# Kernel tuning notes

Measured on AMD Instinct MI355X. Metric: run time of the kernel, lower is better.

The kernel has to match this reference:

```python
import jax, jax.numpy as jnp
import numpy as np

N_NODES = 100000
D_FEAT = 128
N_EDGES = 1600000
N_CLASSES = 32


def setup_inputs() -> dict:
    key = jax.random.key(0)
    k1, k2, k3, k4 = jax.random.split(key, 4)
    x = jax.random.normal(k1, (N_NODES, D_FEAT), dtype=jnp.float32)
    edge_index = jax.random.randint(k2, (2, N_EDGES), 0, N_NODES, dtype=jnp.int64)
    # Linear(input_feat, classes) params (PyTorch default init scale)
    bound = 1.0 / np.sqrt(D_FEAT)
    W = jax.random.uniform(k3, (N_CLASSES, D_FEAT), minval=-bound, maxval=bound, dtype=jnp.float32)
    b = jax.random.uniform(k4, (N_CLASSES,), minval=-bound, maxval=bound, dtype=jnp.float32)
    return {"x": x, "edge_index": edge_index, "W": W, "b": b}


def reference(x, edge_index, W, b):
    # GINConv: out = mlp((1 + eps) * x + sum_{j in N(i)} x_j), eps = 0 (default)
    src, dst = edge_index[0], edge_index[1]
    # gather source features [E, D] and scatter-add into target nodes [N, D]
    agg = jax.ops.segment_sum(x[src], dst, num_segments=N_NODES)
    h = x + agg  # (1 + eps) * x with eps = 0
    # Linear: [N, D] @ [D, C] + [C]
    return h @ W.T + b
```

## Files before the change

kernel.cpp:

```cpp
#include <hip/hip_runtime.h>

#define N_NODES 100000
#define D_FEAT 128
#define N_CLASSES 32
#define BSHIFT 8
#define NB 391
#define EPB 4096
#define CAPB 5120
#define GCAP 1536

typedef __attribute__((ext_vector_type(8))) short short8;
typedef __attribute__((ext_vector_type(4))) float f32x4;

__device__ __forceinline__ unsigned short f2bf(float f) {
  unsigned u = __float_as_uint(f);
  u += 0x7fffu + ((u >> 16) & 1);
  return (unsigned short)(u >> 16);
}

__global__ __launch_bounds__(256) void gin_prep(const float* __restrict__ W,
                                                unsigned short* __restrict__ Wb,
                                                int* __restrict__ gcount) {
  int i = blockIdx.x * 256 + threadIdx.x;
  if (i < D_FEAT * N_CLASSES) Wb[i] = f2bf(W[i]);
  if (i < NB) gcount[i] = 0;
}

__global__ __launch_bounds__(256) void gin_mid(
    const float* __restrict__ x, const unsigned short* __restrict__ Wb,
    float* __restrict__ y,
    const int* __restrict__ src, const int* __restrict__ dst,
    int* __restrict__ gcount, unsigned* __restrict__ bucketed,
    int E, int GBr) {
  __shared__ int cnt[NB];
  __shared__ int cur[NB];
  __shared__ int loff[NB + 1];
  __shared__ int gbase[NB];
  __shared__ int part[256];
  __shared__ unsigned sorted[EPB];
  int tid = threadIdx.x;

  if ((int)blockIdx.x >= GBr) {
    int pb = blockIdx.x - GBr;
    int wave = tid >> 6, lane = tid & 63;
    int node_base = pb * 64 + wave * 16;
    if (node_base >= N_NODES) return;
    int m = lane & 15, quad = lane >> 4;

    short8 bfrag[2][4];
#pragma unroll
    for (int cb = 0; cb < 2; ++cb) {
      const unsigned short* wr = Wb + (cb * 16 + m) * D_FEAT + quad * 8;
#pragma unroll
      for (int ks = 0; ks < 4; ++ks)
        bfrag[cb][ks] = *(const short8*)(wr + ks * 32);
    }

    const float* xr = x + (size_t)(node_base + m) * D_FEAT + quad * 8;
    short8 afrag[4];
#pragma unroll
    for (int ks = 0; ks < 4; ++ks) {
      float4 f0 = *(const float4*)(xr + ks * 32);
      float4 f1 = *(const float4*)(xr + ks * 32 + 4);
      float fl[8] = {f0.x, f0.y, f0.z, f0.w, f1.x, f1.y, f1.z, f1.w};
      short8 a;
#pragma unroll
      for (int j = 0; j < 8; ++j) a[j] = (short)f2bf(fl[j]);
      afrag[ks] = a;
    }

    f32x4 acc0 = {0.f, 0.f, 0.f, 0.f};
    f32x4 acc1 = {0.f, 0.f, 0.f, 0.f};
#pragma unroll
    for (int ks = 0; ks < 4; ++ks) {
      acc0 = __builtin_amdgcn_mfma_f32_16x16x32_bf16(afrag[ks], bfrag[0][ks], acc0, 0, 0, 0);
      acc1 = __builtin_amdgcn_mfma_f32_16x16x32_bf16(afrag[ks], bfrag[1][ks], acc1, 0, 0, 0);
    }

#pragma unroll
    for (int r = 0; r < 4; ++r) {
      int node = node_base + quad * 4 + r;
      y[(size_t)node * N_CLASSES + m] = acc0[r];
      y[(size_t)node * N_CLASSES + 16 + m] = acc1[r];
    }
    return;
  }

  int blk = blockIdx.x;
  for (int i = tid; i < NB; i += 256) {
    cnt[i] = 0;
    cur[i] = 0;
  }
  __syncthreads();
  int base = blk * EPB;
  bool full = (base + EPB <= E);

  int dv[16];
  unsigned sv[16];
  if (full) {
#pragma unroll
    for (int k = 0; k < 16; ++k) dv[k] = dst[base + k * 256 + tid];
#pragma unroll
    for (int k = 0; k < 16; ++k) sv[k] = (unsigned)src[base + k * 256 + tid];
  } else {
#pragma unroll
    for (int k = 0; k < 16; ++k) {
      int e = base + k * 256 + tid;
      dv[k] = (e < E) ? dst[e] : -1;
      sv[k] = (e < E) ? (unsigned)src[e] : 0u;
    }
  }
#pragma unroll
  for (int k = 0; k < 16; ++k)
    if (dv[k] >= 0) atomicAdd(&cnt[dv[k] >> BSHIFT], 1);
  __syncthreads();

  for (int i = tid; i < NB; i += 256) {
    int c = cnt[i];
    gbase[i] = c ? atomicAdd(&gcount[i], c) : 0;
  }
  int i0 = tid * 2;
  int v0 = (i0 < NB) ? cnt[i0] : 0;
  int v1 = (i0 + 1 < NB) ? cnt[i0 + 1] : 0;
  int s0 = v0 + v1;
  part[tid] = s0;
  __syncthreads();
  for (int o = 1; o < 256; o <<= 1) {
    int t = (tid >= o) ? part[tid - o] : 0;
    __syncthreads();
    part[tid] += t;
    __syncthreads();
  }
  int run = part[tid] - s0;
  if (i0 < NB) loff[i0] = run;
  if (i0 + 1 < NB) loff[i0 + 1] = run + v0;
  if (tid == 255) loff[NB] = part[255];
  __syncthreads();

#pragma unroll
  for (int k = 0; k < 16; ++k) {
    if (dv[k] >= 0) {
      int b = dv[k] >> BSHIFT;
      int r = atomicAdd(&cur[b], 1);
      sorted[loff[b] + r] = sv[k] | ((unsigned)(dv[k] & 255) << 17);
    }
  }
  __syncthreads();

  int ltot = loff[NB];
  for (int i = tid; i < ltot; i += 256) {
    int lo = 0, hi = NB;
    while (hi - lo > 1) {
      int md = (lo + hi) >> 1;
      if (loff[md] <= i) lo = md; else hi = md;
    }
    int ga = gbase[lo] + (i - loff[lo]);
    if (ga < CAPB) bucketed[(size_t)lo * CAPB + ga] = sorted[i];
  }
}

__global__ __launch_bounds__(512) void gin_gather_s(
    const int* __restrict__ gcount, const unsigned* __restrict__ bucketed,
    const float* __restrict__ y, const float* __restrict__ bias,
    float* __restrict__ out) {
  __shared__ unsigned sorted[GCAP];
  __shared__ int cnt[64];
  __shared__ int off[65];
  __shared__ int cur[64];
  int tid = threadIdx.x;
  int bk = blockIdx.x >> 2;
  int qq = blockIdx.x & 3;
  int len = gcount[bk];
  if (len > CAPB) len = CAPB;
  const unsigned* bb = bucketed + (size_t)bk * CAPB;
  if (tid < 64) cnt[tid] = 0;
  __syncthreads();
  for (int i = tid; i < len; i += 512) {
    unsigned p = bb[i];
    int n8 = (int)((p >> 17) & 255u);
    if ((n8 >> 6) == qq) atomicAdd(&cnt[n8 & 63], 1);
  }
  __syncthreads();
  if (tid == 0) off[0] = 0;
  if (tid < 64) off[tid + 1] = cnt[tid];
  __syncthreads();
  for (int o = 1; o < 64; o <<= 1) {
    int v = (tid < 64 && tid >= o) ? off[tid + 1 - o] : 0;
    __syncthreads();
    if (tid < 64) off[tid + 1] += v;
    __syncthreads();
  }
  if (tid < 64) cur[tid] = off[tid];
  __syncthreads();
  for (int i = tid; i < len; i += 512) {
    unsigned p = bb[i];
    int n8 = (int)((p >> 17) & 255u);
    if ((n8 >> 6) == qq) {
      int pos = atomicAdd(&cur[n8 & 63], 1);
      if (pos < GCAP) sorted[pos] = p;
    }
  }
  __syncthreads();
  int nl = tid >> 3;
  int q = tid & 7;
  int es = off[nl], ee = off[nl + 1];
  if (ee > GCAP) ee = GCAP;
  if (es > ee) es = ee;
  int node = (bk << 8) + (qq << 6) + nl;
  if (node >= N_NODES) return;
  const float4* y4 = (const float4*)y;
  float4 bq = ((const float4*)bias)[q];
  float4 self = y4[(size_t)node * 8 + q];
  float4 acc;
  acc.x = self.x + bq.x;
  acc.y = self.y + bq.y;
  acc.z = self.z + bq.z;
  acc.w = self.w + bq.w;
  int j = es;
  for (; j + 4 <= ee; j += 4) {
    unsigned s0 = sorted[j] & 0x1FFFF, s1 = sorted[j + 1] & 0x1FFFF;
    unsigned s2 = sorted[j + 2] & 0x1FFFF, s3 = sorted[j + 3] & 0x1FFFF;
    float4 w0 = y4[(size_t)s0 * 8 + q];
    float4 w1 = y4[(size_t)s1 * 8 + q];
    float4 w2 = y4[(size_t)s2 * 8 + q];
    float4 w3 = y4[(size_t)s3 * 8 + q];
    acc.x += w0.x + w1.x + w2.x + w3.x;
    acc.y += w0.y + w1.y + w2.y + w3.y;
    acc.z += w0.z + w1.z + w2.z + w3.z;
    acc.w += w0.w + w1.w + w2.w + w3.w;
  }
  for (; j < ee; ++j) {
    float4 w = y4[(size_t)(sorted[j] & 0x1FFFF) * 8 + q];
    acc.x += w.x; acc.y += w.y; acc.z += w.z; acc.w += w.w;
  }
  ((float4*)out)[(size_t)node * 8 + q] = acc;
}

__global__ __launch_bounds__(256) void gin_bias_init(
    const float* __restrict__ y, const float* __restrict__ b,
    float* __restrict__ out) {
  int gid = blockIdx.x * 256 + threadIdx.x;
  if (gid < N_NODES * N_CLASSES) out[gid] = y[gid] + b[gid & 31];
}
__global__ __launch_bounds__(256) void gin_scatter_fb(
    const int* __restrict__ src, const int* __restrict__ dst,
    const float* __restrict__ y, float* __restrict__ out, int n_edges) {
  long long gid = (long long)blockIdx.x * 256 + threadIdx.x;
  int e = (int)(gid >> 5);
  int c = (int)(gid & 31);
  if (e >= n_edges) return;
  atomicAdd(&out[(size_t)dst[e] * N_CLASSES + c],
            y[(size_t)src[e] * N_CLASSES + c]);
}

extern "C" void kernel_launch(void* const* d_in, const int* in_sizes, int n_in,
                              void* d_out, int out_size, void* d_ws, size_t ws_size,
                              hipStream_t stream) {
  const float* x = (const float*)d_in[0];
  const int* edge_index = (const int*)d_in[1];
  const float* W = (const float*)d_in[2];
  const float* b = (const float*)d_in[3];
  float* out = (float*)d_out;

  int E = in_sizes[1] / 2;
  const int* src = edge_index;
  const int* dst = edge_index + E;

  int GBr = (E + EPB - 1) / EPB;
  int pblocks = (N_NODES + 63) / 64;

  char* ws = (char*)d_ws;
  size_t sz_y = (size_t)N_NODES * N_CLASSES * 4;
  size_t sz_wb = (D_FEAT * N_CLASSES * 2 + 15) & ~15ull;
  size_t sz_bucketed = (((size_t)NB * CAPB * 4) + 15) & ~15ull;
  size_t sz_gcnt = ((size_t)NB * 4 + 15) & ~15ull;

  float* y = (float*)ws;
  unsigned short* Wb = (unsigned short*)(ws + sz_y);
  unsigned* bucketed = (unsigned*)(ws + sz_y + sz_wb);
  int* gcount = (int*)(ws + sz_y + sz_wb + sz_bucketed);
  size_t need = sz_y + sz_wb + sz_bucketed + sz_gcnt;

  bool dense = E > 1750000;

  if (ws_size < need || dense) {
    gin_prep<<<16, 256, 0, stream>>>(W, Wb, (int*)ws);
    gin_mid<<<pblocks, 256, 0, stream>>>(x, Wb, y, src, dst, (int*)ws, (unsigned*)ws, E, 0);
    gin_bias_init<<<(N_NODES * N_CLASSES + 255) / 256, 256, 0, stream>>>(y, b, out);
    long long t2 = (long long)E * N_CLASSES;
    gin_scatter_fb<<<(int)((t2 + 255) / 256), 256, 0, stream>>>(src, dst, y, out, E);
    return;
  }

  gin_prep<<<16, 256, 0, stream>>>(W, Wb, gcount);
  gin_mid<<<GBr + pblocks, 256, 0, stream>>>(x, Wb, y, src, dst, gcount, bucketed, E, GBr);
  gin_gather_s<<<NB * 4, 512, 0, stream>>>(gcount, bucketed, y, b, out);
}
```

Baseline: 155.7 us.

## Scatter bucketed edges directly, stage bucket in LDS, use packed bf16 convert

The bucketing kernel drops its local prefix-sum, LDS sort and binary-search copy-out. Each edge is now written straight to its global bucket slot using the per-block base plus its atomic rank, which cuts barriers and LDS use but makes the global writes less coalesced. The gather kernel keeps the bucket in a 20KB LDS stage buffer so its second pass does not re-read global memory, at the cost of more LDS per block and possibly lower occupancy. The projection path replaces the software float-to-bf16 rounding with the hardware packed convert instruction.

```diff
diff --git a/kernel.cpp b/kernel.cpp
--- a/kernel.cpp
+++ b/kernel.cpp
@@ -18,6 +18,12 @@
   return (unsigned short)(u >> 16);
 }
 
+__device__ __forceinline__ unsigned cvtpk(float lo, float hi) {
+  unsigned r;
+  asm("v_cvt_pk_bf16_f32 %0, %1, %2" : "=v"(r) : "v"(lo), "v"(hi));
+  return r;
+}
+
 __global__ __launch_bounds__(256) void gin_prep(const float* __restrict__ W,
                                                 unsigned short* __restrict__ Wb,
                                                 int* __restrict__ gcount) {
@@ -34,10 +40,7 @@
     int E, int GBr) {
   __shared__ int cnt[NB];
   __shared__ int cur[NB];
-  __shared__ int loff[NB + 1];
   __shared__ int gbase[NB];
-  __shared__ int part[256];
-  __shared__ unsigned sorted[EPB];
   int tid = threadIdx.x;
 
   if ((int)blockIdx.x >= GBr) {
@@ -62,11 +65,12 @@
     for (int ks = 0; ks < 4; ++ks) {
       float4 f0 = *(const float4*)(xr + ks * 32);
       float4 f1 = *(const float4*)(xr + ks * 32 + 4);
-      float fl[8] = {f0.x, f0.y, f0.z, f0.w, f1.x, f1.y, f1.z, f1.w};
-      short8 a;
-#pragma unroll
-      for (int j = 0; j < 8; ++j) a[j] = (short)f2bf(fl[j]);
-      afrag[ks] = a;
+      union { uint4 u; short8 s; } au;
+      au.u.x = cvtpk(f0.x, f0.y);
+      au.u.y = cvtpk(f0.z, f0.w);
+      au.u.z = cvtpk(f1.x, f1.y);
+      au.u.w = cvtpk(f1.z, f1.w);
+      afrag[ks] = au.s;
     }
 
     f32x4 acc0 = {0.f, 0.f, 0.f, 0.f};
@@ -119,22 +123,6 @@
     int c = cnt[i];
     gbase[i] = c ? atomicAdd(&gcount[i], c) : 0;
   }
-  int i0 = tid * 2;
-  int v0 = (i0 < NB) ? cnt[i0] : 0;
-  int v1 = (i0 + 1 < NB) ? cnt[i0 + 1] : 0;
-  int s0 = v0 + v1;
-  part[tid] = s0;
-  __syncthreads();
-  for (int o = 1; o < 256; o <<= 1) {
-    int t = (tid >= o) ? part[tid - o] : 0;
-    __syncthreads();
-    part[tid] += t;
-    __syncthreads();
-  }
-  int run = part[tid] - s0;
-  if (i0 < NB) loff[i0] = run;
-  if (i0 + 1 < NB) loff[i0 + 1] = run + v0;
-  if (tid == 255) loff[NB] = part[255];
   __syncthreads();
 
 #pragma unroll
@@ -142,20 +130,10 @@
     if (dv[k] >= 0) {
       int b = dv[k] >> BSHIFT;
       int r = atomicAdd(&cur[b], 1);
-      sorted[loff[b] + r] = sv[k] | ((unsigned)(dv[k] & 255) << 17);
-    }
-  }
-  __syncthreads();
-
-  int ltot = loff[NB];
-  for (int i = tid; i < ltot; i += 256) {
-    int lo = 0, hi = NB;
-    while (hi - lo > 1) {
-      int md = (lo + hi) >> 1;
-      if (loff[md] <= i) lo = md; else hi = md;
-    }
-    int ga = gbase[lo] + (i - loff[lo]);
-    if (ga < CAPB) bucketed[(size_t)lo * CAPB + ga] = sorted[i];
+      int ga = gbase[b] + r;
+      if (ga < CAPB)
+        bucketed[(size_t)b * CAPB + ga] = sv[k] | ((unsigned)(dv[k] & 255) << 17);
+    }
   }
 }
 
@@ -163,6 +141,7 @@
     const int* __restrict__ gcount, const unsigned* __restrict__ bucketed,
     const float* __restrict__ y, const float* __restrict__ bias,
     float* __restrict__ out) {
+  __shared__ unsigned stage[CAPB];
   __shared__ unsigned sorted[GCAP];
   __shared__ int cnt[64];
   __shared__ int off[65];
@@ -177,6 +156,7 @@
   __syncthreads();
   for (int i = tid; i < len; i += 512) {
     unsigned p = bb[i];
+    stage[i] = p;
     int n8 = (int)((p >> 17) & 255u);
     if ((n8 >> 6) == qq) atomicAdd(&cnt[n8 & 63], 1);
   }
@@ -193,7 +173,7 @@
   if (tid < 64) cur[tid] = off[tid];
   __syncthreads();
   for (int i = tid; i < len; i += 512) {
-    unsigned p = bb[i];
+    unsigned p = stage[i];
     int n8 = (int)((p >> 17) & 255u);
     if ((n8 >> 6) == qq) {
       int pos = atomicAdd(&cur[n8 & 63], 1);
```

New measurement: 153.0 us. About the same (-1.7%).
